# Kernel optimization log

Measured on AMD Instinct MI355X. Metric: run time of the kernel, lower is better.

Reference implementation:

```python
import jax, jax.numpy as jnp
import numpy as np

DIM = 512
WINDOW = 8
HEADS = 16
HEAD_DIM = DIM // HEADS
SIGMA = 0.39
B = 2048
N = WINDOW * WINDOW


def gaussian_kernel(window_size, sigma):
    """Row-normalised Gaussian attention mask K_sigma (M^2 x M^2)."""
    c = jnp.arange(window_size, dtype=jnp.float32)
    gy, gx = jnp.meshgrid(c, c, indexing='ij')
    pos = jnp.stack([gy.flatten(), gx.flatten()], -1)  # [M^2, 2]
    diff = pos[None, :, :] - pos[:, None, :]           # [M^2, M^2, 2]
    K = jnp.exp(-(diff ** 2).sum(-1) / (2.0 * sigma ** 2))
    return K / K.sum(-1, keepdims=True)


def setup_inputs() -> dict:
    key = jax.random.key(0)
    k1, k2, k3, k4, k5 = jax.random.split(key, 5)
    x = jax.random.normal(k1, (B, N, DIM), dtype=jnp.float32)
    # spectral_norm at inference is just a fixed scaling of the weight; we
    # model the (already-normalised) weights as plain dense params.
    w_qkv = jax.random.normal(k2, (DIM, 3 * DIM), dtype=jnp.float32) * (DIM ** -0.5)
    b_qkv = jax.random.normal(k3, (3 * DIM,), dtype=jnp.float32) * 0.02
    w_proj = jax.random.normal(k4, (DIM, DIM), dtype=jnp.float32) * (DIM ** -0.5)
    b_proj = jax.random.normal(k5, (DIM,), dtype=jnp.float32) * 0.02
    return {"x": x, "w_qkv": w_qkv, "b_qkv": b_qkv, "w_proj": w_proj, "b_proj": b_proj}


def reference(x, w_qkv, b_qkv, w_proj, b_proj):
    Bb, Nn, C = x.shape
    scale = HEAD_DIM ** -0.5
    qkv = (x @ w_qkv + b_qkv).reshape(Bb, Nn, 3, HEADS, HEAD_DIM)
    qkv = jnp.transpose(qkv, (2, 0, 3, 1, 4))  # [3, B, H, N, D]
    q, k, v = qkv[0], qkv[1], qkv[2]
    attn = jnp.einsum('bhnd,bhmd->bhnm', q, k) * scale  # [B, H, N, N]
    K_s = gaussian_kernel(WINDOW, SIGMA)                 # [N, N]
    attn = jax.nn.softmax(attn * K_s, axis=-1)
    out = jnp.einsum('bhnm,bhmd->bhnd', attn, v)         # [B, H, N, D]
    out = jnp.transpose(out, (0, 2, 1, 3)).reshape(Bb, Nn, C)
    return out @ w_proj + b_proj
```

## Files before the change

### kernel.cpp

```cpp
#include <hip/hip_runtime.h>
#include <hip/hip_bf16.h>
#include <stdint.h>

typedef __bf16 bf16;
typedef __bf16 bf16x8 __attribute__((ext_vector_type(8)));
typedef float f32x4 __attribute__((ext_vector_type(4)));
typedef unsigned short u16t;
typedef unsigned int u32t;

#define MFMA16(a, b, c) __builtin_amdgcn_mfma_f32_16x16x32_bf16((a), (b), (c), 0, 0, 0)

typedef const void __attribute__((address_space(1))) cg_void;
typedef void __attribute__((address_space(3))) lds_void;
#define GLL16(g, l) __builtin_amdgcn_global_load_lds((cg_void*)(g), (lds_void*)(l), 16, 0, 0)
#define VWAIT(n) asm volatile("s_waitcnt vmcnt(" #n ")" ::: "memory")

#define OFF_FLAG   0
#define OFF_BQKV   256
#define OFF_BPROJ  6400
#define OFF_WQKVT  8448
#define OFF_WPROJT 1581312
#define OFF_QKV    2105600
#define OFF_ATTN   404758784
#define OFF_XB     404758784


__global__ __launch_bounds__(256) void k_detect(const u16t* x, u32t* flag) {
    __shared__ int cnt;
    if (threadIdx.x == 0) cnt = 0;
    __syncthreads();
    u16t h = x[threadIdx.x * 2];
    int e = (h >> 7) & 0xFF;
    int ok = (h == 0) || (e >= 100 && e <= 134);
    atomicAdd(&cnt, ok);
    __syncthreads();
    if (threadIdx.x == 0) flag[0] = (cnt >= 200) ? 1u : 0u;
}

__global__ __launch_bounds__(256) void k_cvt(const float* x, bf16* xb, const u32t* flagp) {
    if (flagp[0]) return;
    const size_t TOT = (size_t)131072 * 512;
    size_t i = (size_t)(blockIdx.x * 256 + threadIdx.x) * 8;
    const size_t stride = (size_t)gridDim.x * 256 * 8;
    for (; i < TOT; i += stride) {
        float4 v0 = *(const float4*)(x + i);
        float4 v1 = *(const float4*)(x + i + 4);
        bf16x8 h;
        h[0] = (bf16)v0.x; h[1] = (bf16)v0.y; h[2] = (bf16)v0.z; h[3] = (bf16)v0.w;
        h[4] = (bf16)v1.x; h[5] = (bf16)v1.y; h[6] = (bf16)v1.z; h[7] = (bf16)v1.w;
        *(bf16x8*)(xb + i) = h;
    }
}

template <int N, bool PERM>
__global__ __launch_bounds__(256) void k_trans(const void* W, bf16* Wt, const u32t* flagp) {
    __shared__ float T[64][65];
    const int isbf = (int)flagp[0];
    const int n0 = blockIdx.x * 64, k0 = blockIdx.y * 64;
    const int t = threadIdx.x;
    const int lc = t & 63, lr = t >> 6;
#pragma unroll
    for (int rr = 0; rr < 16; ++rr) {
        int row = rr * 4 + lr;
        int col = n0 + lc;
        int srcc = col;
        if (PERM) {
            int h = col / 96, r = col % 96;
            srcc = (r >> 5) * 512 + h * 32 + (r & 31);
        }
        size_t g = (size_t)(k0 + row) * N + srcc;
        float v = isbf ? (float)((const bf16*)W)[g] : ((const float*)W)[g];
        T[row][lc] = v;
    }
    __syncthreads();
#pragma unroll
    for (int rr = 0; rr < 16; ++rr) {
        int row = rr * 4 + lr;
        Wt[(size_t)(n0 + row) * 512 + k0 + lc] = (bf16)T[lc][row];
    }
}

__global__ __launch_bounds__(256) void k_bias(const void* b_qkv, const void* b_proj,
                                              const u32t* flagp, char* ws) {
    float* bq = (float*)(ws + OFF_BQKV);
    float* bp = (float*)(ws + OFF_BPROJ);
    const int isbf = (int)flagp[0];
    int gid = blockIdx.x * 256 + threadIdx.x;
    if (gid < 1536) {
        int h = gid / 96, r = gid % 96;
        int src = (r >> 5) * 512 + h * 32 + (r & 31);
        bq[gid] = isbf ? (float)((const bf16*)b_qkv)[src] : ((const float*)b_qkv)[src];
    } else if (gid < 2048) {
        int o = gid - 1536;
        bp[o] = isbf ? (float)((const bf16*)b_proj)[o] : ((const float*)b_proj)[o];
    }
}

template <int NTOT>
__global__ __launch_bounds__(512, 2) void k_gemm(const void* Ax, const bf16* Axb, const bf16* Bt,
                                                 const float* bias, void* Cp,
                                                 const u32t* flagp, int omode) {
    __shared__ __align__(16) u16t As[2 * 16384];
    __shared__ __align__(16) u16t Bs[2 * 16384];
    constexpr int NBN = NTOT / 256;
    const int isbf = (int)flagp[0];
    const int out_bf16 = (omode == 1) || isbf;
    const bf16* Ab = isbf ? (const bf16*)Ax : Axb;

    const int t = threadIdx.x;
    const int w = t >> 6, lane = t & 63;
    const int ln = lane & 15, qd = lane >> 4;
    const int wm = w >> 2, wn = w & 3;

    const int flat = blockIdx.x;
    const int xcd = flat & 7, slot = flat >> 3;
    const int n_idx = slot % NBN, grp = slot / NBN;
    const int m0 = (grp * 8 + xcd) * 256;
    const int n0 = n_idx * 256;

    const int l8 = lane >> 3, pc = lane & 7;
    const int cs8 = (pc ^ l8) * 8;
    u32t aoff[2][2], boff[2][2];
    int adst[2][2], bdst[2][2];
#pragma unroll
    for (int s = 0; s < 2; ++s)
#pragma unroll
        for (int q2 = 0; q2 < 2; ++q2) {
            int rA = q2 * 128 + s * 64 + w * 8;
            aoff[s][q2] = (u32t)(m0 + rA + l8) * 512 + cs8;
            adst[s][q2] = rA * 64;
            int rB = (q2 * 2 + (w >> 2)) * 64 + s * 32 + (w & 3) * 8;
            boff[s][q2] = (u32t)(n0 + rB + l8) * 512 + cs8;
            bdst[s][q2] = rB * 64;
        }

    const int p0 = (qd ^ (ln & 7)) * 8;
    int abase[4], bbase[2];
#pragma unroll
    for (int i = 0; i < 4; ++i) abase[i] = (wm * 128 + i * 16 + ln) * 64 + p0;
#pragma unroll
    for (int j = 0; j < 2; ++j) bbase[j] = (wn * 64 + j * 16 + ln) * 64 + p0;

    f32x4 acc[8][4];
    f32x4 zero = {0.f, 0.f, 0.f, 0.f};
#pragma unroll
    for (int i = 0; i < 8; ++i)
#pragma unroll
        for (int j = 0; j < 4; ++j) acc[i][j] = zero;

    auto stageA = [&](int s, int buf, int kt) {
#pragma unroll
        for (int q2 = 0; q2 < 2; ++q2)
            GLL16(Ab + aoff[s][q2] + kt * 64, &As[buf * 16384 + adst[s][q2]]);
    };
    auto stageB = [&](int s, int buf, int kt) {
#pragma unroll
        for (int q2 = 0; q2 < 2; ++q2)
            GLL16(Bt + boff[s][q2] + kt * 64, &Bs[buf * 16384 + bdst[s][q2]]);
    };

#define PH(BUF, QM, QN, STG, WAITOP)                                             \
    {                                                                            \
        bf16x8 af[4][2], bv[2][2];                                               \
        const u16t* Ap = &As[(BUF) * 16384 + (QM) * 4096];                       \
        const u16t* Bp = &Bs[(BUF) * 16384 + (QN) * 2048];                       \
        _Pragma("unroll") for (int i = 0; i < 4; ++i) {                          \
            af[i][0] = *(const bf16x8*)(const void*)&Ap[abase[i]];               \
            af[i][1] = *(const bf16x8*)(const void*)&Ap[abase[i] ^ 32];          \
        }                                                                        \
        _Pragma("unroll") for (int j = 0; j < 2; ++j) {                          \
            bv[j][0] = *(const bf16x8*)(const void*)&Bp[bbase[j]];               \
            bv[j][1] = *(const bf16x8*)(const void*)&Bp[bbase[j] ^ 32];          \
        }                                                                        \
        STG;                                                                     \
        WAITOP;                                                                  \
        __builtin_amdgcn_s_barrier();                                            \
        __builtin_amdgcn_s_setprio(1);                                           \
        _Pragma("unroll") for (int i = 0; i < 4; ++i)                            \
            _Pragma("unroll") for (int j = 0; j < 2; ++j) {                      \
                acc[(QM) * 4 + i][(QN) * 2 + j] =                                \
                    MFMA16(af[i][0], bv[j][0], acc[(QM) * 4 + i][(QN) * 2 + j]); \
                acc[(QM) * 4 + i][(QN) * 2 + j] =                                \
                    MFMA16(af[i][1], bv[j][1], acc[(QM) * 4 + i][(QN) * 2 + j]); \
            }                                                                    \
        __builtin_amdgcn_s_setprio(0);                                           \
        __builtin_amdgcn_s_barrier();                                            \
    }

    stageA(0, 0, 0);
    stageB(0, 0, 0);
    stageB(1, 0, 0);
    stageA(1, 0, 0);
    VWAIT(4);
    __builtin_amdgcn_s_barrier();

    for (int kt = 0; kt < 7; ++kt) {
        const int buf = kt & 1, nb = buf ^ 1, k1 = kt + 1;
        PH(buf, 0, 0, stageA(0, nb, k1), VWAIT(4));
        PH(buf, 0, 1, stageB(0, nb, k1), VWAIT(4));
        PH(buf, 1, 0, stageB(1, nb, k1), VWAIT(6));
        PH(buf, 1, 1, stageA(1, nb, k1), VWAIT(4));
    }
    PH(1, 0, 0, (void)0, VWAIT(2));
    PH(1, 0, 1, (void)0, VWAIT(0));
    PH(1, 1, 0, (void)0, (void)0);
    PH(1, 1, 1, (void)0, (void)0);
#undef PH

    float bj[4];
#pragma unroll
    for (int j = 0; j < 4; ++j) bj[j] = bias[n0 + wn * 64 + j * 16 + ln];

    if (out_bf16) {
        bf16* C = (bf16*)Cp;
#pragma unroll
        for (int i = 0; i < 8; ++i)
#pragma unroll
            for (int j = 0; j < 4; ++j)
#pragma unroll
                for (int rr = 0; rr < 4; ++rr) {
                    size_t row = (size_t)m0 + wm * 128 + i * 16 + qd * 4 + rr;
                    int col = n0 + wn * 64 + j * 16 + ln;
                    C[row * NTOT + col] = (bf16)(acc[i][j][rr] + bj[j]);
                }
    } else {
        float* C = (float*)Cp;
#pragma unroll
        for (int i = 0; i < 8; ++i)
#pragma unroll
            for (int j = 0; j < 4; ++j)
#pragma unroll
                for (int rr = 0; rr < 4; ++rr) {
                    size_t row = (size_t)m0 + wm * 128 + i * 16 + qd * 4 + rr;
                    int col = n0 + wn * 64 + j * 16 + ln;
                    C[row * NTOT + col] = acc[i][j][rr] + bj[j];
                }
    }
}

__global__ __launch_bounds__(512, 2) void k_fused(const void* Ax, const bf16* Axb,
                                                  const bf16* Bt, const float* bias,
                                                  bf16* attnout, const u32t* flagp) {
    __shared__ __align__(16) u16t pool[57344];
    const int isbf = (int)flagp[0];
    const bf16* Ab = isbf ? (const bf16*)Ax : Axb;

    const int t = threadIdx.x;
    const int w = t >> 6, lane = t & 63;
    const int ln = lane & 15, qd = lane >> 4, q8 = qd * 8;
    const int wm = w >> 2, wn = w & 3;

    const int flat = blockIdx.x;
    const int xcd = flat & 7, slot = flat >> 3;
    const int n_idx = slot & 7, grp = slot >> 3;
    const int m0 = (grp * 8 + xcd) * 256;
    const int n0 = n_idx * 192;

    const int l8 = lane >> 3, pc = lane & 7;
    const int cs8 = (pc ^ l8) * 8;
    u32t aoff[4], boff[3];
    int adst[4], bdst[3];
#pragma unroll
    for (int qa = 0; qa < 4; ++qa) {
        int row = qa * 64 + w * 8 + l8;
        aoff[qa] = (u32t)(m0 + row) * 512 + cs8;
        adst[qa] = (qa * 512 + w * 64) * 8;
    }
#pragma unroll
    for (int qb = 0; qb < 3; ++qb) {
        int row = qb * 64 + w * 8 + l8;
        boff[qb] = (u32t)(n0 + row) * 512 + cs8;
        bdst[qb] = (qb * 512 + w * 64) * 8;
    }

    const int swz = (qd ^ (ln & 7)) * 8;
    int afo[2][4], bfo[3];
#pragma unroll
    for (int qm = 0; qm < 2; ++qm)
#pragma unroll
        for (int i = 0; i < 4; ++i)
            afo[qm][i] = (wm * 128 + qm * 64 + i * 16 + ln) * 64 + swz;
#pragma unroll
    for (int j = 0; j < 3; ++j) bfo[j] = (wn * 48 + j * 16 + ln) * 64 + swz;

    f32x4 acc[8][3];
    f32x4 zero = {0.f, 0.f, 0.f, 0.f};
#pragma unroll
    for (int i = 0; i < 8; ++i)
#pragma unroll
        for (int j = 0; j < 3; ++j) acc[i][j] = zero;

    auto stA = [&](int qa, int buf, int kt) {
        GLL16(Ab + aoff[qa] + kt * 64, &pool[buf * 16384 + adst[qa]]);
    };
    auto stB = [&](int qb, int buf, int kt) {
        GLL16(Bt + boff[qb] + kt * 64, &pool[32768 + buf * 12288 + bdst[qb]]);
    };

#define PHF(BUF, QM, KK, STG, WAITOP)                                           \
    {                                                                           \
        bf16x8 af[4], bv[3];                                                    \
        _Pragma("unroll") for (int i = 0; i < 4; ++i)                           \
            af[i] = *(const bf16x8*)(const void*)                               \
                &pool[(BUF) * 16384 + (afo[QM][i] ^ ((KK) * 32))];              \
        _Pragma("unroll") for (int j = 0; j < 3; ++j)                           \
            bv[j] = *(const bf16x8*)(const void*)                               \
                &pool[32768 + (BUF) * 12288 + (bfo[j] ^ ((KK) * 32))];          \
        STG;                                                                    \
        WAITOP;                                                                 \
        __builtin_amdgcn_s_barrier();                                           \
        __builtin_amdgcn_s_setprio(1);                                          \
        _Pragma("unroll") for (int i = 0; i < 4; ++i)                           \
            _Pragma("unroll") for (int j = 0; j < 3; ++j)                       \
                acc[(QM) * 4 + i][j] = MFMA16(af[i], bv[j], acc[(QM) * 4 + i][j]); \
        __builtin_amdgcn_s_setprio(0);                                          \
        __builtin_amdgcn_s_barrier();                                           \
    }

    stA(0, 0, 0); stA(2, 0, 0);
    stB(0, 0, 0); stB(1, 0, 0); stB(2, 0, 0);
    stA(1, 0, 0); stA(3, 0, 0);
    VWAIT(2);
    __builtin_amdgcn_s_barrier();

    for (int kt = 0; kt < 7; ++kt) {
        const int buf = kt & 1, nb = buf ^ 1, k1 = kt + 1;
        PHF(buf, 0, 0, (stA(0, nb, k1), stA(2, nb, k1)), (void)0);
        PHF(buf, 0, 1, (stB(0, nb, k1), stB(1, nb, k1)), VWAIT(4));
        PHF(buf, 1, 0, (stB(2, nb, k1), stA(1, nb, k1)), (void)0);
        PHF(buf, 1, 1, (stA(3, nb, k1)), VWAIT(2));
    }
    PHF(1, 0, 0, (void)0, (void)0);
    PHF(1, 0, 1, (void)0, VWAIT(0));
    PHF(1, 1, 0, (void)0, (void)0);
    PHF(1, 1, 1, (void)0, (void)0);
#undef PHF

    float bj[3];
#pragma unroll
    for (int j = 0; j < 3; ++j) bj[j] = bias[n0 + wn * 48 + j * 16 + ln];

#pragma unroll
    for (int i = 0; i < 8; ++i) {
        int win = wm * 2 + (i >> 2);
#pragma unroll
        for (int j = 0; j < 3; ++j) {
            int base = wn * 48 + j * 16;
            int hl = base >= 96;
            int bb = base - hl * 96;
            int part = bb >> 5;
            int d = (bb & 31) + ln;
            int patch = (win * 2 + hl) * 6656;
#pragma unroll
            for (int rr = 0; rr < 4; ++rr) {
                int tok = (i & 3) * 16 + qd * 4 + rr;
                bf16 val = (bf16)(acc[i][j][rr] + bj[j]);
                int idx;
                if (part == 2)
                    idx = patch + 4608 + tok * 32 +
                          (((d >> 3) ^ (((tok >> 3) ^ tok) & 3)) << 3) + (d & 7);
                else
                    idx = patch + part * 2048 + tok * 32 +
                          (((d >> 3) ^ ((tok >> 1) & 3)) << 3) + (d & 7);
                *(bf16*)&pool[idx] = val;
            }
        }
    }
    __syncthreads();

    {
        const int patch = w * 6656;
        const int win = w >> 1, hl = w & 1;
        const int hcol = (n_idx * 2 + hl) * 32;
        const int qswz = (qd ^ ((ln >> 1) & 3)) * 8;

        bf16x8 aq[4], bk[4];
#pragma unroll
        for (int i = 0; i < 4; ++i)
            aq[i] = *(const bf16x8*)(const void*)&pool[patch + (i * 16 + ln) * 32 + qswz];
#pragma unroll
        for (int j = 0; j < 4; ++j)
            bk[j] = *(const bf16x8*)(const void*)&pool[patch + 2048 + (j * 16 + ln) * 32 + qswz];

        f32x4 zro = {0.f, 0.f, 0.f, 0.f};
        f32x4 s[4][4];
#pragma unroll
        for (int i = 0; i < 4; ++i)
#pragma unroll
            for (int j = 0; j < 4; ++j) s[i][j] = MFMA16(aq[i], bk[j], zro);

        const float INV2S2 = 3.28731097961867f;
        {
            int c = lane & 7;
            float S1 = 0.f;
#pragma unroll
            for (int c2 = 0; c2 < 8; ++c2) {
                int dd = c - c2;
                S1 += __expf(-(float)(dd * dd) * INV2S2);
            }
            float invS1 = 1.0f / S1;
            const int ymb = ln >> 3, xm = ln & 7, yq = qd >> 1, xq = (qd & 1) * 4;
            float FY[4][4], FX[4];
#pragma unroll
            for (int i = 0; i < 4; ++i) {
                int yn = 2 * i + yq;
                float g = __shfl(invS1, yn, 64);
#pragma unroll
                for (int j = 0; j < 4; ++j) {
                    int dy = yn - (2 * j + ymb);
                    FY[i][j] = __expf(-(float)(dy * dy) * INV2S2) * g;
                }
            }
#pragma unroll
            for (int rr = 0; rr < 4; ++rr) {
                int xn = xq + rr;
                int dx = xn - xm;
                FX[rr] = __expf(-(float)(dx * dx) * INV2S2) * __shfl(invS1, xn, 64);
            }

            const float SCALE = 0.17677669529663687f;
#pragma unroll
            for (int i = 0; i < 4; ++i)
#pragma unroll
                for (int rr = 0; rr < 4; ++rr) {
                    float lj[4];
                    float mx = -1e30f;
#pragma unroll
                    for (int j = 0; j < 4; ++j) {
                        lj[j] = s[i][j][rr] * SCALE * FY[i][j] * FX[rr];
                        mx = fmaxf(mx, lj[j]);
                    }
                    mx = fmaxf(mx, __shfl_xor(mx, 1));
                    mx = fmaxf(mx, __shfl_xor(mx, 2));
                    mx = fmaxf(mx, __shfl_xor(mx, 4));
                    mx = fmaxf(mx, __shfl_xor(mx, 8));
                    float sum = 0.f;
#pragma unroll
                    for (int j = 0; j < 4; ++j) {
                        lj[j] = __expf(lj[j] - mx);
                        sum += lj[j];
                    }
                    sum += __shfl_xor(sum, 1);
                    sum += __shfl_xor(sum, 2);
                    sum += __shfl_xor(sum, 4);
                    sum += __shfl_xor(sum, 8);
                    float inv = 1.0f / sum;
                    int n = i * 16 + qd * 4 + rr;
#pragma unroll
                    for (int j = 0; j < 4; ++j) {
                        bf16 pv = (bf16)(lj[j] * inv);
                        *(bf16*)&pool[patch + n * 72 + j * 16 + ln] = pv;
                    }
                }
        }

        f32x4 o[4][2];
#pragma unroll
        for (int i = 0; i < 4; ++i) {
            o[i][0] = zro;
            o[i][1] = zro;
        }
#pragma unroll
        for (int kc = 0; kc < 64; kc += 32) {
            bf16x8 bv2[2];
#pragma unroll
            for (int j2 = 0; j2 < 2; ++j2) {
                int cc = j2 * 2 + (ln >> 3);
#pragma unroll
                for (int jj = 0; jj < 8; ++jj) {
                    int rv = kc + q8 + jj;
                    bv2[j2][jj] = *(const bf16*)&pool[patch + 4608 + rv * 32 +
                                                     ((cc ^ (((rv >> 3) ^ rv) & 3)) << 3) + (ln & 7)];
                }
            }
#pragma unroll
            for (int i = 0; i < 4; ++i) {
                bf16x8 ap = *(const bf16x8*)(const void*)&pool[patch + (i * 16 + ln) * 72 + kc + q8];
#pragma unroll
                for (int j2 = 0; j2 < 2; ++j2) o[i][j2] = MFMA16(ap, bv2[j2], o[i][j2]);
            }
        }
#pragma unroll
        for (int i = 0; i < 4; ++i)
#pragma unroll
            for (int j2 = 0; j2 < 2; ++j2)
#pragma unroll
                for (int rr = 0; rr < 4; ++rr)
                    attnout[((size_t)m0 + win * 64 + i * 16 + qd * 4 + rr) * 512 +
                            hcol + j2 * 16 + ln] = (bf16)(o[i][j2][rr]);
    }
}

extern "C" void kernel_launch(void* const* d_in, const int* in_sizes, int n_in,
                              void* d_out, int out_size, void* d_ws, size_t ws_size,
                              hipStream_t stream) {
    const void* x = d_in[0];
    const void* w_qkv = d_in[1];
    const void* b_qkv = d_in[2];
    const void* w_proj = d_in[3];
    const void* b_proj = d_in[4];
    char* ws = (char*)d_ws;
    u32t* flag = (u32t*)(ws + OFF_FLAG);
    bf16* wqkvT = (bf16*)(ws + OFF_WQKVT);
    bf16* wprojT = (bf16*)(ws + OFF_WPROJT);
    float* bq = (float*)(ws + OFF_BQKV);
    float* bp = (float*)(ws + OFF_BPROJ);
    bf16* attnout = (bf16*)(ws + OFF_QKV);
    bf16* xb = (bf16*)(ws + OFF_XB);

    k_detect<<<1, 256, 0, stream>>>((const u16t*)x, flag);
    k_cvt<<<2048, 256, 0, stream>>>((const float*)x, xb, flag);
    k_trans<1536, true><<<dim3(24, 8), 256, 0, stream>>>(w_qkv, wqkvT, flag);
    k_trans<512, false><<<dim3(8, 8), 256, 0, stream>>>(w_proj, wprojT, flag);
    k_bias<<<8, 256, 0, stream>>>(b_qkv, b_proj, flag, ws);
    k_fused<<<4096, 512, 0, stream>>>(x, xb, wqkvT, bq, attnout, flag);
    k_gemm<512><<<1024, 512, 0, stream>>>((const void*)attnout, attnout, wprojT, bp, d_out, flag, 2);
}
```

Before: 953.2 us.

## Restructure fused QKV+attention kernel to one window per block, weights from global

The fused QKV projection plus attention kernel is reorganised so each block handles one 64-token window and half the heads, with each wave owning one head's full Q/K/V columns. Only the activation tile is staged in LDS, in two K-halves. Weight fragments are read straight from global memory into registers, and the software-pipelined double buffering is dropped. This removes the shared 256x192 tile and the block-wide barrier before attention, but loses double buffering and relies on L2 for weight reuse, since every block rereads a 96-column weight slice.

```diff
diff --git a/kernel.cpp b/kernel.cpp
--- a/kernel.cpp
+++ b/kernel.cpp
@@ -238,149 +238,118 @@
     }
 }
 
-__global__ __launch_bounds__(512, 2) void k_fused(const void* Ax, const bf16* Axb,
-                                                  const bf16* Bt, const float* bias,
-                                                  bf16* attnout, const u32t* flagp) {
-    __shared__ __align__(16) u16t pool[57344];
+__global__ __launch_bounds__(512, 2) void k_mega(const void* Ax, const bf16* Axb,
+                                                 const bf16* Bt, const float* bias,
+                                                 bf16* attnout, const u32t* flagp) {
+    __shared__ __align__(16) u16t Axs[16384];
+    __shared__ __align__(16) u16t patch[8][6656];
     const int isbf = (int)flagp[0];
     const bf16* Ab = isbf ? (const bf16*)Ax : Axb;
 
     const int t = threadIdx.x;
     const int w = t >> 6, lane = t & 63;
     const int ln = lane & 15, qd = lane >> 4, q8 = qd * 8;
-    const int wm = w >> 2, wn = w & 3;
 
     const int flat = blockIdx.x;
     const int xcd = flat & 7, slot = flat >> 3;
-    const int n_idx = slot & 7, grp = slot >> 3;
-    const int m0 = (grp * 8 + xcd) * 256;
-    const int n0 = n_idx * 192;
-
-    const int l8 = lane >> 3, pc = lane & 7;
-    const int cs8 = (pc ^ l8) * 8;
-    u32t aoff[4], boff[3];
-    int adst[4], bdst[3];
-#pragma unroll
-    for (int qa = 0; qa < 4; ++qa) {
-        int row = qa * 64 + w * 8 + l8;
-        aoff[qa] = (u32t)(m0 + row) * 512 + cs8;
-        adst[qa] = (qa * 512 + w * 64) * 8;
-    }
-#pragma unroll
-    for (int qb = 0; qb < 3; ++qb) {
-        int row = qb * 64 + w * 8 + l8;
-        boff[qb] = (u32t)(n0 + row) * 512 + cs8;
-        bdst[qb] = (qb * 512 + w * 64) * 8;
-    }
-
-    const int swz = (qd ^ (ln & 7)) * 8;
-    int afo[2][4], bfo[3];
-#pragma unroll
-    for (int qm = 0; qm < 2; ++qm)
-#pragma unroll
-        for (int i = 0; i < 4; ++i)
-            afo[qm][i] = (wm * 128 + qm * 64 + i * 16 + ln) * 64 + swz;
-#pragma unroll
-    for (int j = 0; j < 3; ++j) bfo[j] = (wn * 48 + j * 16 + ln) * 64 + swz;
-
-    f32x4 acc[8][3];
+    const int hb = slot & 1;
+    const int win = xcd * 256 + (slot >> 1);
+    const int g = hb * 8 + w;
+    const size_t xbase = (size_t)win * 64 * 512;
+
+    u32t asrc[4];
+#pragma unroll
+    for (int q = 0; q < 4; ++q) {
+        int row = w * 8 + q * 2 + (lane >> 5);
+        asrc[q] = (u32t)row * 512 + (u32t)(((lane & 31) ^ (row & 7)) * 8);
+    }
+
+    const bf16* bp6[6];
+#pragma unroll
+    for (int j = 0; j < 6; ++j)
+        bp6[j] = Bt + (size_t)(g * 96 + j * 16 + ln) * 512 + q8;
+
+    f32x4 acc[4][6];
     f32x4 zero = {0.f, 0.f, 0.f, 0.f};
 #pragma unroll
-    for (int i = 0; i < 8; ++i)
-#pragma unroll
-        for (int j = 0; j < 3; ++j) acc[i][j] = zero;
-
-    auto stA = [&](int qa, int buf, int kt) {
-        GLL16(Ab + aoff[qa] + kt * 64, &pool[buf * 16384 + adst[qa]]);
-    };
-    auto stB = [&](int qb, int buf, int kt) {
-        GLL16(Bt + boff[qb] + kt * 64, &pool[32768 + buf * 12288 + bdst[qb]]);
-    };
-
-#define PHF(BUF, QM, KK, STG, WAITOP)                                           \
-    {                                                                           \
-        bf16x8 af[4], bv[3];                                                    \
-        _Pragma("unroll") for (int i = 0; i < 4; ++i)                           \
-            af[i] = *(const bf16x8*)(const void*)                               \
-                &pool[(BUF) * 16384 + (afo[QM][i] ^ ((KK) * 32))];              \
-        _Pragma("unroll") for (int j = 0; j < 3; ++j)                           \
-            bv[j] = *(const bf16x8*)(const void*)                               \
-                &pool[32768 + (BUF) * 12288 + (bfo[j] ^ ((KK) * 32))];          \
-        STG;                                                                    \
-        WAITOP;                                                                 \
-        __builtin_amdgcn_s_barrier();                                           \
-        __builtin_amdgcn_s_setprio(1);                                          \
-        _Pragma("unroll") for (int i = 0; i < 4; ++i)                           \
-            _Pragma("unroll") for (int j = 0; j < 3; ++j)                       \
-                acc[(QM) * 4 + i][j] = MFMA16(af[i], bv[j], acc[(QM) * 4 + i][j]); \
-        __builtin_amdgcn_s_setprio(0);                                          \
-        __builtin_amdgcn_s_barrier();                                           \
-    }
-
-    stA(0, 0, 0); stA(2, 0, 0);
-    stB(0, 0, 0); stB(1, 0, 0); stB(2, 0, 0);
-    stA(1, 0, 0); stA(3, 0, 0);
-    VWAIT(2);
-    __builtin_amdgcn_s_barrier();
-
-    for (int kt = 0; kt < 7; ++kt) {
-        const int buf = kt & 1, nb = buf ^ 1, k1 = kt + 1;
-        PHF(buf, 0, 0, (stA(0, nb, k1), stA(2, nb, k1)), (void)0);
-        PHF(buf, 0, 1, (stB(0, nb, k1), stB(1, nb, k1)), VWAIT(4));
-        PHF(buf, 1, 0, (stB(2, nb, k1), stA(1, nb, k1)), (void)0);
-        PHF(buf, 1, 1, (stA(3, nb, k1)), VWAIT(2));
-    }
-    PHF(1, 0, 0, (void)0, (void)0);
-    PHF(1, 0, 1, (void)0, VWAIT(0));
-    PHF(1, 1, 0, (void)0, (void)0);
-    PHF(1, 1, 1, (void)0, (void)0);
-#undef PHF
-
-    float bj[3];
-#pragma unroll
-    for (int j = 0; j < 3; ++j) bj[j] = bias[n0 + wn * 48 + j * 16 + ln];
-
-#pragma unroll
-    for (int i = 0; i < 8; ++i) {
-        int win = wm * 2 + (i >> 2);
-#pragma unroll
-        for (int j = 0; j < 3; ++j) {
-            int base = wn * 48 + j * 16;
-            int hl = base >= 96;
-            int bb = base - hl * 96;
-            int part = bb >> 5;
-            int d = (bb & 31) + ln;
-            int patch = (win * 2 + hl) * 6656;
+    for (int i = 0; i < 4; ++i)
+#pragma unroll
+        for (int j = 0; j < 6; ++j) acc[i][j] = zero;
+
+#pragma unroll
+    for (int kh = 0; kh < 2; ++kh) {
+        if (kh) __builtin_amdgcn_s_barrier();
+#pragma unroll
+        for (int q = 0; q < 4; ++q)
+            GLL16(Ab + xbase + kh * 256 + asrc[q], &Axs[(w * 8 + q * 2) * 256]);
+        VWAIT(0);
+        __builtin_amdgcn_s_barrier();
+#pragma unroll
+        for (int kt = 0; kt < 4; ++kt) {
+            const int kg = kh * 4 + kt;
+            bf16x8 bfr[6][2];
+#pragma unroll
+            for (int j = 0; j < 6; ++j) {
+                bfr[j][0] = *(const bf16x8*)(bp6[j] + kg * 64);
+                bfr[j][1] = *(const bf16x8*)(bp6[j] + kg * 64 + 32);
+            }
+#pragma unroll
+            for (int kk = 0; kk < 2; ++kk) {
+                bf16x8 af[4];
+#pragma unroll
+                for (int i = 0; i < 4; ++i) {
+                    int row = i * 16 + ln;
+                    int chunk = kt * 8 + kk * 4 + qd;
+                    af[i] = *(const bf16x8*)(const void*)
+                        &Axs[row * 256 + (chunk ^ (row & 7)) * 8];
+                }
+                __builtin_amdgcn_s_setprio(1);
+#pragma unroll
+                for (int i = 0; i < 4; ++i)
+#pragma unroll
+                    for (int j = 0; j < 6; ++j)
+                        acc[i][j] = MFMA16(af[i], bfr[j][kk], acc[i][j]);
+                __builtin_amdgcn_s_setprio(0);
+            }
+        }
+    }
+
+    float bj[6];
+#pragma unroll
+    for (int j = 0; j < 6; ++j) bj[j] = bias[g * 96 + j * 16 + ln];
+    u16t* pw = patch[w];
+#pragma unroll
+    for (int i = 0; i < 4; ++i)
+#pragma unroll
+        for (int j = 0; j < 6; ++j) {
+            int part = j >> 1;
+            int d = (j & 1) * 16 + ln;
 #pragma unroll
             for (int rr = 0; rr < 4; ++rr) {
-                int tok = (i & 3) * 16 + qd * 4 + rr;
+                int tok = i * 16 + qd * 4 + rr;
                 bf16 val = (bf16)(acc[i][j][rr] + bj[j]);
                 int idx;
                 if (part == 2)
-                    idx = patch + 4608 + tok * 32 +
+                    idx = 4608 + tok * 32 +
                           (((d >> 3) ^ (((tok >> 3) ^ tok) & 3)) << 3) + (d & 7);
                 else
-                    idx = patch + part * 2048 + tok * 32 +
+                    idx = part * 2048 + tok * 32 +
                           (((d >> 3) ^ ((tok >> 1) & 3)) << 3) + (d & 7);
-                *(bf16*)&pool[idx] = val;
-            }
-        }
-    }
-    __syncthreads();
+                *(bf16*)&pw[idx] = val;
+            }
+        }
 
     {
-        const int patch = w * 6656;
-        const int win = w >> 1, hl = w & 1;
-        const int hcol = (n_idx * 2 + hl) * 32;
+        const int hcol = g * 32;
         const int qswz = (qd ^ ((ln >> 1) & 3)) * 8;
 
         bf16x8 aq[4], bk[4];
 #pragma unroll
         for (int i = 0; i < 4; ++i)
-            aq[i] = *(const bf16x8*)(const void*)&pool[patch + (i * 16 + ln) * 32 + qswz];
+            aq[i] = *(const bf16x8*)(const void*)&pw[(i * 16 + ln) * 32 + qswz];
 #pragma unroll
         for (int j = 0; j < 4; ++j)
-            bk[j] = *(const bf16x8*)(const void*)&pool[patch + 2048 + (j * 16 + ln) * 32 + qswz];
+            bk[j] = *(const bf16x8*)(const void*)&pw[2048 + (j * 16 + ln) * 32 + qswz];
 
         f32x4 zro = {0.f, 0.f, 0.f, 0.f};
         f32x4 s[4][4];
@@ -404,11 +373,11 @@
 #pragma unroll
             for (int i = 0; i < 4; ++i) {
                 int yn = 2 * i + yq;
-                float g = __shfl(invS1, yn, 64);
+                float gg = __shfl(invS1, yn, 64);
 #pragma unroll
                 for (int j = 0; j < 4; ++j) {
                     int dy = yn - (2 * j + ymb);
-                    FY[i][j] = __expf(-(float)(dy * dy) * INV2S2) * g;
+                    FY[i][j] = __expf(-(float)(dy * dy) * INV2S2) * gg;
                 }
             }
 #pragma unroll
@@ -449,7 +418,7 @@
 #pragma unroll
                     for (int j = 0; j < 4; ++j) {
                         bf16 pv = (bf16)(lj[j] * inv);
-                        *(bf16*)&pool[patch + n * 72 + j * 16 + ln] = pv;
+                        *(bf16*)&pw[n * 72 + j * 16 + ln] = pv;
                     }
                 }
         }
@@ -469,13 +438,13 @@
 #pragma unroll
                 for (int jj = 0; jj < 8; ++jj) {
                     int rv = kc + q8 + jj;
-                    bv2[j2][jj] = *(const bf16*)&pool[patch + 4608 + rv * 32 +
-                                                     ((cc ^ (((rv >> 3) ^ rv) & 3)) << 3) + (ln & 7)];
+                    bv2[j2][jj] = *(const bf16*)&pw[4608 + rv * 32 +
+                                                   ((cc ^ (((rv >> 3) ^ rv) & 3)) << 3) + (ln & 7)];
                 }
             }
 #pragma unroll
             for (int i = 0; i < 4; ++i) {
-                bf16x8 ap = *(const bf16x8*)(const void*)&pool[patch + (i * 16 + ln) * 72 + kc + q8];
+                bf16x8 ap = *(const bf16x8*)(const void*)&pw[(i * 16 + ln) * 72 + kc + q8];
 #pragma unroll
                 for (int j2 = 0; j2 < 2; ++j2) o[i][j2] = MFMA16(ap, bv2[j2], o[i][j2]);
             }
@@ -486,7 +455,7 @@
             for (int j2 = 0; j2 < 2; ++j2)
 #pragma unroll
                 for (int rr = 0; rr < 4; ++rr)
-                    attnout[((size_t)m0 + win * 64 + i * 16 + qd * 4 + rr) * 512 +
+                    attnout[((size_t)win * 64 + i * 16 + qd * 4 + rr) * 512 +
                             hcol + j2 * 16 + ln] = (bf16)(o[i][j2][rr]);
     }
 }
@@ -513,6 +482,6 @@
     k_trans<1536, true><<<dim3(24, 8), 256, 0, stream>>>(w_qkv, wqkvT, flag);
     k_trans<512, false><<<dim3(8, 8), 256, 0, stream>>>(w_proj, wprojT, flag);
     k_bias<<<8, 256, 0, stream>>>(b_qkv, b_proj, flag, ws);
-    k_fused<<<4096, 512, 0, stream>>>(x, xb, wqkvT, bq, attnout, flag);
+    k_mega<<<4096, 512, 0, stream>>>(x, xb, wqkvT, bq, attnout, flag);
     k_gemm<512><<<1024, 512, 0, stream>>>((const void*)attnout, attnout, wprojT, bp, d_out, flag, 2);
 }
```

Measured after the change: 1.103 ms. 15.7% more time.
